# Kernel optimization log

Measured on AMD Instinct MI355X. Metric: run time of the kernel, lower is better.

## Reference

```python
import jax, jax.numpy as jnp
import numpy as np

B, N, A, M = 65536, 256, 64, 128  # frames, atoms, align atoms, nn atoms


def setup_inputs() -> dict:
    key = jax.random.key(0)
    k1, k2, k3, k4 = jax.random.split(key, 4)
    traj = jax.random.normal(k1, (B, N, 3), dtype=jnp.float32)
    ref_pos = jax.random.normal(k2, (N, 3), dtype=jnp.float32)
    align_idx = jnp.sort(jax.random.randint(k3, (A,), 0, N))
    nn_idx = jnp.sort(jax.random.randint(k4, (M,), 0, N))
    return {"traj": traj, "ref_pos": ref_pos, "align_idx": align_idx, "nn_idx": nn_idx}


def reference(traj, ref_pos, align_idx, nn_idx):
    # Reference structure: select alignment atoms and remove centroid (done once in __init__)
    ref_x = ref_pos[align_idx]                      # [A, 3]
    ref_x = ref_x - ref_x.mean(axis=0, keepdims=True)

    # Kabsch alignment per frame
    sel = traj[:, align_idx, :]                     # [B, A, 3]
    x_c = sel.mean(axis=1, keepdims=True)           # [B, 1, 3]
    x_notran = sel - x_c                            # [B, A, 3]
    # prod = x_notran^T @ ref_x -> [B, 3, 3]
    prod = jnp.einsum('bni,nj->bij', x_notran, ref_x)
    u, s, vh = jnp.linalg.svd(prod)                 # batched 3x3 SVD
    # proper-rotation sign correction (detached in original)
    sign = jax.lax.stop_gradient(jnp.sign(jnp.linalg.det(u @ vh)))  # [B]
    ones = jnp.ones_like(sign)
    d = jnp.stack([ones, ones, sign], axis=-1)      # [B, 3] diagonal of correction
    rot = (u * d[:, None, :]) @ vh                  # [B, 3, 3]

    # apply translation + rotation to ALL atoms
    aligned = jnp.einsum('bni,bij->bnj', traj - x_c, rot)  # [B, N, 3]

    # select NN input atoms and flatten
    return aligned[:, nn_idx, :].reshape(traj.shape[0], -1)  # [B, M*3]
```

## Files before the change

kernel.cpp:

```cpp
#include <hip/hip_runtime.h>

#define NB 65536
#define NATOM 256
#define NA 64
#define NM 128
#define TRAJ_SZ (NB*NATOM*3)
#define REF_SZ  (NATOM*3)
#define SLOT_F  384
#define ROW_F   (NATOM*3)

__device__ __forceinline__ float bf2f(unsigned short u) {
    union { unsigned int i; float f; } v; v.i = ((unsigned int)u) << 16; return v.f;
}
__device__ __forceinline__ float wave_sum(float v) {
    #pragma unroll
    for (int m = 1; m < 64; m <<= 1) v += __shfl_xor(v, m, 64);
    return v;
}
__device__ __forceinline__ float wave_max(float v) {
    #pragma unroll
    for (int m = 1; m < 64; m <<= 1) v = fmaxf(v, __shfl_xor(v, m, 64));
    return v;
}

__device__ __forceinline__ int detect_f32(const unsigned short* __restrict__ traj_u) {
    int lane = threadIdx.x & 63;
    float mx = fabsf(bf2f(traj_u[2 * lane]));
    mx = wave_max(mx);
    return (mx > 0.5f && mx < 100.f) ? 0 : 1;
}

__global__ __launch_bounds__(256) void k_fused(const unsigned short* __restrict__ traj_u,
                                               const unsigned short* __restrict__ refp_u,
                                               const int* __restrict__ align_idx,
                                               const int* __restrict__ nn_idx,
                                               float* __restrict__ out) {
    __shared__ float rowbuf[4][ROW_F];
    __shared__ float outbuf[4][SLOT_F];
    int lane = threadIdx.x & 63;
    int wid  = threadIdx.x >> 6;
    long batch = ((long)blockIdx.x << 2) + wid;
    int isf32 = detect_f32(traj_u);

    if (isf32) {
        const float4* src = (const float4*)((const float*)traj_u + batch * ROW_F);
        float4* dst = (float4*)rowbuf[wid];
        dst[lane]       = src[lane];
        dst[lane + 64]  = src[lane + 64];
        dst[lane + 128] = src[lane + 128];
    } else {
        const unsigned int* src = (const unsigned int*)(traj_u + batch * ROW_F);
        float2* dst = (float2*)rowbuf[wid];
        #pragma unroll
        for (int k = 0; k < 6; ++k) {
            unsigned int u = src[lane + 64 * k];
            dst[lane + 64 * k] = make_float2(bf2f((unsigned short)(u & 0xffffu)),
                                             bf2f((unsigned short)(u >> 16)));
        }
    }
    __syncthreads();

    int aidx = align_idx[lane];
    float r0, r1, r2;
    if (isf32) {
        const float* rp = (const float*)refp_u;
        r0 = rp[aidx*3+0]; r1 = rp[aidx*3+1]; r2 = rp[aidx*3+2];
    } else {
        r0 = bf2f(refp_u[aidx*3+0]); r1 = bf2f(refp_u[aidx*3+1]); r2 = bf2f(refp_u[aidx*3+2]);
    }
    float x0 = rowbuf[wid][aidx*3+0];
    float x1 = rowbuf[wid][aidx*3+1];
    float x2 = rowbuf[wid][aidx*3+2];
    r0 -= wave_sum(r0) * (1.f/64.f);
    r1 -= wave_sum(r1) * (1.f/64.f);
    r2 -= wave_sum(r2) * (1.f/64.f);
    float p00 = wave_sum(x0*r0), p01 = wave_sum(x0*r1), p02 = wave_sum(x0*r2);
    float p10 = wave_sum(x1*r0), p11 = wave_sum(x1*r1), p12 = wave_sum(x1*r2);
    float p20 = wave_sum(x2*r0), p21 = wave_sum(x2*r1), p22 = wave_sum(x2*r2);
    float xc0 = wave_sum(x0) * (1.f/64.f);
    float xc1 = wave_sum(x1) * (1.f/64.f);
    float xc2 = wave_sum(x2) * (1.f/64.f);

    float s00 = p00*p00 + p10*p10 + p20*p20;
    float s01 = p00*p01 + p10*p11 + p20*p21;
    float s02 = p00*p02 + p10*p12 + p20*p22;
    float s11 = p01*p01 + p11*p11 + p21*p21;
    float s12 = p01*p02 + p11*p12 + p21*p22;
    float s22 = p02*p02 + p12*p12 + p22*p22;
    float v00=1.f,v01=0.f,v02=0.f, v10=0.f,v11=1.f,v12=0.f, v20=0.f,v21=0.f,v22=1.f;
#define JROT(SPP,SQQ,SPQ,SRP,SRQ,VA,VB,VC,VD,VE,VF) { \
    float apq = SPQ; \
    if (apq != 0.0f) { \
        float tau = (SQQ - SPP) / (2.0f*apq); \
        float t = (tau >= 0.0f ? 1.0f : -1.0f) / (fabsf(tau) + sqrtf(1.0f + tau*tau)); \
        float c = 1.0f / sqrtf(1.0f + t*t); \
        float sn = t*c; \
        SPP -= t*apq; SQQ += t*apq; SPQ = 0.0f; \
        float tp = SRP; SRP = c*tp - sn*SRQ; SRQ = sn*tp + c*SRQ; \
        tp = VA; VA = c*tp - sn*VB; VB = sn*tp + c*VB; \
        tp = VC; VC = c*tp - sn*VD; VD = sn*tp + c*VD; \
        tp = VE; VE = c*tp - sn*VF; VF = sn*tp + c*VF; \
    } }
    #pragma unroll
    for (int sweep = 0; sweep < 5; ++sweep) {
        JROT(s00,s11,s01, s02,s12, v00,v01, v10,v11, v20,v21);
        JROT(s00,s22,s02, s01,s12, v00,v02, v10,v12, v20,v22);
        JROT(s11,s22,s12, s01,s02, v01,v02, v11,v12, v21,v22);
    }
#undef JROT
    float v1x,v1y,v1z, v2x,v2y,v2z;
    if (s00 <= s11 && s00 <= s22) {
        v1x=v01; v1y=v11; v1z=v21;  v2x=v02; v2y=v12; v2z=v22;
    } else if (s11 <= s22) {
        v1x=v02; v1y=v12; v1z=v22;  v2x=v00; v2y=v10; v2z=v20;
    } else {
        v1x=v00; v1y=v10; v1z=v20;  v2x=v01; v2y=v11; v2z=v21;
    }
    float u1x = p00*v1x + p01*v1y + p02*v1z;
    float u1y = p10*v1x + p11*v1y + p12*v1z;
    float u1z = p20*v1x + p21*v1y + p22*v1z;
    float inv = 1.0f / sqrtf(u1x*u1x + u1y*u1y + u1z*u1z);
    u1x*=inv; u1y*=inv; u1z*=inv;
    float u2x = p00*v2x + p01*v2y + p02*v2z;
    float u2y = p10*v2x + p11*v2y + p12*v2z;
    float u2z = p20*v2x + p21*v2y + p22*v2z;
    float d = u2x*u1x + u2y*u1y + u2z*u1z;
    u2x -= d*u1x; u2y -= d*u1y; u2z -= d*u1z;
    inv = 1.0f / sqrtf(u2x*u2x + u2y*u2y + u2z*u2z);
    u2x*=inv; u2y*=inv; u2z*=inv;
    float u3x = u1y*u2z - u1z*u2y;
    float u3y = u1z*u2x - u1x*u2z;
    float u3z = u1x*u2y - u1y*u2x;
    float v3x = v1y*v2z - v1z*v2y;
    float v3y = v1z*v2x - v1x*v2z;
    float v3z = v1x*v2y - v1y*v2x;
    float r00 = u1x*v1x + u2x*v2x + u3x*v3x;
    float r01 = u1x*v1y + u2x*v2y + u3x*v3y;
    float r02 = u1x*v1z + u2x*v2z + u3x*v3z;
    float r10 = u1y*v1x + u2y*v2x + u3y*v3x;
    float r11 = u1y*v1y + u2y*v2y + u3y*v3y;
    float r12 = u1y*v1z + u2y*v2z + u3y*v3z;
    float r20 = u1z*v1x + u2z*v2x + u3z*v3x;
    float r21 = u1z*v1y + u2z*v2y + u3z*v3y;
    float r22 = u1z*v1z + u2z*v2z + u3z*v3z;

    #pragma unroll
    for (int h = 0; h < 2; ++h) {
        int m = lane + 64 * h;
        int nidx = nn_idx[m];
        float y0 = rowbuf[wid][nidx*3+0] - xc0;
        float y1 = rowbuf[wid][nidx*3+1] - xc1;
        float y2 = rowbuf[wid][nidx*3+2] - xc2;
        outbuf[wid][3*m+0] = y0*r00 + y1*r10 + y2*r20;
        outbuf[wid][3*m+1] = y0*r01 + y1*r11 + y2*r21;
        outbuf[wid][3*m+2] = y0*r02 + y1*r12 + y2*r22;
    }
    __syncthreads();
    const float4* ob = (const float4*)outbuf[wid];
    float4* og = (float4*)(out + batch * SLOT_F);
    og[lane] = ob[lane];
    if (lane < 32) og[64 + lane] = ob[64 + lane];
}

extern "C" void kernel_launch(void* const* d_in, const int* in_sizes, int n_in,
                              void* d_out, int out_size, void* d_ws, size_t ws_size,
                              hipStream_t stream) {
    const unsigned short* traj = (const unsigned short*)d_in[0];
    const unsigned short* refp = (const unsigned short*)d_in[1];
    const int* align_idx = (const int*)d_in[2];
    const int* nn_idx    = (const int*)d_in[3];
    for (int i = 0; i < n_in; ++i) {
        if      (in_sizes[i] == TRAJ_SZ) traj      = (const unsigned short*)d_in[i];
        else if (in_sizes[i] == REF_SZ)  refp      = (const unsigned short*)d_in[i];
        else if (in_sizes[i] == NA)      align_idx = (const int*)d_in[i];
        else if (in_sizes[i] == NM)      nn_idx    = (const int*)d_in[i];
    }
    float* out = (float*)d_out;

    k_fused<<<NB/4, 256, 0, stream>>>(traj, refp, align_idx, nn_idx, out);
}
```

Baseline: 374.4 us.

## Batch eight frames per block and run the SVD once per frame across lanes

Each block now processes eight frames instead of four. Each wave reduces the cross-covariance for two frames, and the partial sums are staged in shared memory. A single lane per frame then runs the Jacobi eigen-solve and builds the rotation, where before all 64 lanes of a wave repeated the same 3x3 solve. The rotated output is written back in place over the row buffer and stored cooperatively by the whole block. The aim is to remove the redundant per-lane SVD work and the separate output buffer. The cost is two more block-wide barriers and a solve stage that runs on only eight lanes while the other waves sit idle.

Result: faster. 318.2 us (-15.0%).

```diff
diff --git a/kernel.cpp b/kernel.cpp
--- a/kernel.cpp
+++ b/kernel.cpp
@@ -8,6 +8,7 @@
 #define REF_SZ  (NATOM*3)
 #define SLOT_F  384
 #define ROW_F   (NATOM*3)
+#define NBB     8
 
 __device__ __forceinline__ float bf2f(unsigned short u) {
     union { unsigned int i; float f; } v; v.i = ((unsigned int)u) << 16; return v.f;
@@ -35,27 +36,27 @@
                                                const int* __restrict__ align_idx,
                                                const int* __restrict__ nn_idx,
                                                float* __restrict__ out) {
-    __shared__ float rowbuf[4][ROW_F];
-    __shared__ float outbuf[4][SLOT_F];
-    int lane = threadIdx.x & 63;
-    int wid  = threadIdx.x >> 6;
-    long batch = ((long)blockIdx.x << 2) + wid;
+    __shared__ float rowbuf[NBB][ROW_F];
+    __shared__ float pbuf[NBB][12];
+    int tid  = threadIdx.x;
+    int lane = tid & 63;
+    int wid  = tid >> 6;
+    long bbase = (long)blockIdx.x * NBB;
     int isf32 = detect_f32(traj_u);
 
     if (isf32) {
-        const float4* src = (const float4*)((const float*)traj_u + batch * ROW_F);
-        float4* dst = (float4*)rowbuf[wid];
-        dst[lane]       = src[lane];
-        dst[lane + 64]  = src[lane + 64];
-        dst[lane + 128] = src[lane + 128];
+        const float2* src = (const float2*)((const float*)traj_u + bbase * ROW_F);
+        float2* dst = (float2*)&rowbuf[0][0];
+        #pragma unroll
+        for (int k = 0; k < 12; ++k) dst[tid + 256*k] = src[tid + 256*k];
     } else {
-        const unsigned int* src = (const unsigned int*)(traj_u + batch * ROW_F);
-        float2* dst = (float2*)rowbuf[wid];
+        const unsigned int* src = (const unsigned int*)(traj_u + bbase * ROW_F);
+        float2* dst = (float2*)&rowbuf[0][0];
         #pragma unroll
-        for (int k = 0; k < 6; ++k) {
-            unsigned int u = src[lane + 64 * k];
-            dst[lane + 64 * k] = make_float2(bf2f((unsigned short)(u & 0xffffu)),
-                                             bf2f((unsigned short)(u >> 16)));
+        for (int k = 0; k < 12; ++k) {
+            unsigned int u = src[tid + 256*k];
+            dst[tid + 256*k] = make_float2(bf2f((unsigned short)(u & 0xffffu)),
+                                           bf2f((unsigned short)(u >> 16)));
         }
     }
     __syncthreads();
@@ -68,98 +69,142 @@
     } else {
         r0 = bf2f(refp_u[aidx*3+0]); r1 = bf2f(refp_u[aidx*3+1]); r2 = bf2f(refp_u[aidx*3+2]);
     }
-    float x0 = rowbuf[wid][aidx*3+0];
-    float x1 = rowbuf[wid][aidx*3+1];
-    float x2 = rowbuf[wid][aidx*3+2];
     r0 -= wave_sum(r0) * (1.f/64.f);
     r1 -= wave_sum(r1) * (1.f/64.f);
     r2 -= wave_sum(r2) * (1.f/64.f);
-    float p00 = wave_sum(x0*r0), p01 = wave_sum(x0*r1), p02 = wave_sum(x0*r2);
-    float p10 = wave_sum(x1*r0), p11 = wave_sum(x1*r1), p12 = wave_sum(x1*r2);
-    float p20 = wave_sum(x2*r0), p21 = wave_sum(x2*r1), p22 = wave_sum(x2*r2);
-    float xc0 = wave_sum(x0) * (1.f/64.f);
-    float xc1 = wave_sum(x1) * (1.f/64.f);
-    float xc2 = wave_sum(x2) * (1.f/64.f);
-
-    float s00 = p00*p00 + p10*p10 + p20*p20;
-    float s01 = p00*p01 + p10*p11 + p20*p21;
-    float s02 = p00*p02 + p10*p12 + p20*p22;
-    float s11 = p01*p01 + p11*p11 + p21*p21;
-    float s12 = p01*p02 + p11*p12 + p21*p22;
-    float s22 = p02*p02 + p12*p12 + p22*p22;
-    float v00=1.f,v01=0.f,v02=0.f, v10=0.f,v11=1.f,v12=0.f, v20=0.f,v21=0.f,v22=1.f;
+    #pragma unroll
+    for (int s = 0; s < 2; ++s) {
+        int lb = 2*wid + s;
+        const float* row = rowbuf[lb];
+        float x0 = row[aidx*3+0];
+        float x1 = row[aidx*3+1];
+        float x2 = row[aidx*3+2];
+        float p00 = wave_sum(x0*r0), p01 = wave_sum(x0*r1), p02 = wave_sum(x0*r2);
+        float p10 = wave_sum(x1*r0), p11 = wave_sum(x1*r1), p12 = wave_sum(x1*r2);
+        float p20 = wave_sum(x2*r0), p21 = wave_sum(x2*r1), p22 = wave_sum(x2*r2);
+        float xc0 = wave_sum(x0) * (1.f/64.f);
+        float xc1 = wave_sum(x1) * (1.f/64.f);
+        float xc2 = wave_sum(x2) * (1.f/64.f);
+        if (lane == 0) {
+            pbuf[lb][0] = p00; pbuf[lb][1] = p01; pbuf[lb][2]  = p02;
+            pbuf[lb][3] = p10; pbuf[lb][4] = p11; pbuf[lb][5]  = p12;
+            pbuf[lb][6] = p20; pbuf[lb][7] = p21; pbuf[lb][8]  = p22;
+            pbuf[lb][9] = xc0; pbuf[lb][10] = xc1; pbuf[lb][11] = xc2;
+        }
+    }
+    __syncthreads();
+
+    if (tid < NBB) {
+        float* w = pbuf[tid];
+        float p00=w[0], p01=w[1], p02=w[2];
+        float p10=w[3], p11=w[4], p12=w[5];
+        float p20=w[6], p21=w[7], p22=w[8];
+        float s00 = p00*p00 + p10*p10 + p20*p20;
+        float s01 = p00*p01 + p10*p11 + p20*p21;
+        float s02 = p00*p02 + p10*p12 + p20*p22;
+        float s11 = p01*p01 + p11*p11 + p21*p21;
+        float s12 = p01*p02 + p11*p12 + p21*p22;
+        float s22 = p02*p02 + p12*p12 + p22*p22;
+        float v00=1.f,v01=0.f,v02=0.f, v10=0.f,v11=1.f,v12=0.f, v20=0.f,v21=0.f,v22=1.f;
 #define JROT(SPP,SQQ,SPQ,SRP,SRQ,VA,VB,VC,VD,VE,VF) { \
-    float apq = SPQ; \
-    if (apq != 0.0f) { \
-        float tau = (SQQ - SPP) / (2.0f*apq); \
-        float t = (tau >= 0.0f ? 1.0f : -1.0f) / (fabsf(tau) + sqrtf(1.0f + tau*tau)); \
-        float c = 1.0f / sqrtf(1.0f + t*t); \
-        float sn = t*c; \
-        SPP -= t*apq; SQQ += t*apq; SPQ = 0.0f; \
-        float tp = SRP; SRP = c*tp - sn*SRQ; SRQ = sn*tp + c*SRQ; \
-        tp = VA; VA = c*tp - sn*VB; VB = sn*tp + c*VB; \
-        tp = VC; VC = c*tp - sn*VD; VD = sn*tp + c*VD; \
-        tp = VE; VE = c*tp - sn*VF; VF = sn*tp + c*VF; \
-    } }
-    #pragma unroll
-    for (int sweep = 0; sweep < 5; ++sweep) {
-        JROT(s00,s11,s01, s02,s12, v00,v01, v10,v11, v20,v21);
-        JROT(s00,s22,s02, s01,s12, v00,v02, v10,v12, v20,v22);
-        JROT(s11,s22,s12, s01,s02, v01,v02, v11,v12, v21,v22);
-    }
+        float apq = SPQ; \
+        if (apq != 0.0f) { \
+            float tau = (SQQ - SPP) / (2.0f*apq); \
+            float t = (tau >= 0.0f ? 1.0f : -1.0f) / (fabsf(tau) + sqrtf(1.0f + tau*tau)); \
+            float c = 1.0f / sqrtf(1.0f + t*t); \
+            float sn = t*c; \
+            SPP -= t*apq; SQQ += t*apq; SPQ = 0.0f; \
+            float tp = SRP; SRP = c*tp - sn*SRQ; SRQ = sn*tp + c*SRQ; \
+            tp = VA; VA = c*tp - sn*VB; VB = sn*tp + c*VB; \
+            tp = VC; VC = c*tp - sn*VD; VD = sn*tp + c*VD; \
+            tp = VE; VE = c*tp - sn*VF; VF = sn*tp + c*VF; \
+        } }
+        #pragma unroll
+        for (int sweep = 0; sweep < 5; ++sweep) {
+            JROT(s00,s11,s01, s02,s12, v00,v01, v10,v11, v20,v21);
+            JROT(s00,s22,s02, s01,s12, v00,v02, v10,v12, v20,v22);
+            JROT(s11,s22,s12, s01,s02, v01,v02, v11,v12, v21,v22);
+        }
 #undef JROT
-    float v1x,v1y,v1z, v2x,v2y,v2z;
-    if (s00 <= s11 && s00 <= s22) {
-        v1x=v01; v1y=v11; v1z=v21;  v2x=v02; v2y=v12; v2z=v22;
-    } else if (s11 <= s22) {
-        v1x=v02; v1y=v12; v1z=v22;  v2x=v00; v2y=v10; v2z=v20;
-    } else {
-        v1x=v00; v1y=v10; v1z=v20;  v2x=v01; v2y=v11; v2z=v21;
-    }
-    float u1x = p00*v1x + p01*v1y + p02*v1z;
-    float u1y = p10*v1x + p11*v1y + p12*v1z;
-    float u1z = p20*v1x + p21*v1y + p22*v1z;
-    float inv = 1.0f / sqrtf(u1x*u1x + u1y*u1y + u1z*u1z);
-    u1x*=inv; u1y*=inv; u1z*=inv;
-    float u2x = p00*v2x + p01*v2y + p02*v2z;
-    float u2y = p10*v2x + p11*v2y + p12*v2z;
-    float u2z = p20*v2x + p21*v2y + p22*v2z;
-    float d = u2x*u1x + u2y*u1y + u2z*u1z;
-    u2x -= d*u1x; u2y -= d*u1y; u2z -= d*u1z;
-    inv = 1.0f / sqrtf(u2x*u2x + u2y*u2y + u2z*u2z);
-    u2x*=inv; u2y*=inv; u2z*=inv;
-    float u3x = u1y*u2z - u1z*u2y;
-    float u3y = u1z*u2x - u1x*u2z;
-    float u3z = u1x*u2y - u1y*u2x;
-    float v3x = v1y*v2z - v1z*v2y;
-    float v3y = v1z*v2x - v1x*v2z;
-    float v3z = v1x*v2y - v1y*v2x;
-    float r00 = u1x*v1x + u2x*v2x + u3x*v3x;
-    float r01 = u1x*v1y + u2x*v2y + u3x*v3y;
-    float r02 = u1x*v1z + u2x*v2z + u3x*v3z;
-    float r10 = u1y*v1x + u2y*v2x + u3y*v3x;
-    float r11 = u1y*v1y + u2y*v2y + u3y*v3y;
-    float r12 = u1y*v1z + u2y*v2z + u3y*v3z;
-    float r20 = u1z*v1x + u2z*v2x + u3z*v3x;
-    float r21 = u1z*v1y + u2z*v2y + u3z*v3y;
-    float r22 = u1z*v1z + u2z*v2z + u3z*v3z;
-
-    #pragma unroll
-    for (int h = 0; h < 2; ++h) {
-        int m = lane + 64 * h;
-        int nidx = nn_idx[m];
-        float y0 = rowbuf[wid][nidx*3+0] - xc0;
-        float y1 = rowbuf[wid][nidx*3+1] - xc1;
-        float y2 = rowbuf[wid][nidx*3+2] - xc2;
-        outbuf[wid][3*m+0] = y0*r00 + y1*r10 + y2*r20;
-        outbuf[wid][3*m+1] = y0*r01 + y1*r11 + y2*r21;
-        outbuf[wid][3*m+2] = y0*r02 + y1*r12 + y2*r22;
-    }
-    __syncthreads();
-    const float4* ob = (const float4*)outbuf[wid];
-    float4* og = (float4*)(out + batch * SLOT_F);
-    og[lane] = ob[lane];
-    if (lane < 32) og[64 + lane] = ob[64 + lane];
+        float v1x,v1y,v1z, v2x,v2y,v2z;
+        if (s00 <= s11 && s00 <= s22) {
+            v1x=v01; v1y=v11; v1z=v21;  v2x=v02; v2y=v12; v2z=v22;
+        } else if (s11 <= s22) {
+            v1x=v02; v1y=v12; v1z=v22;  v2x=v00; v2y=v10; v2z=v20;
+        } else {
+            v1x=v00; v1y=v10; v1z=v20;  v2x=v01; v2y=v11; v2z=v21;
+        }
+        float u1x = p00*v1x + p01*v1y + p02*v1z;
+        float u1y = p10*v1x + p11*v1y + p12*v1z;
+        float u1z = p20*v1x + p21*v1y + p22*v1z;
+        float inv = 1.0f / sqrtf(u1x*u1x + u1y*u1y + u1z*u1z);
+        u1x*=inv; u1y*=inv; u1z*=inv;
+        float u2x = p00*v2x + p01*v2y + p02*v2z;
+        float u2y = p10*v2x + p11*v2y + p12*v2z;
+        float u2z = p20*v2x + p21*v2y + p22*v2z;
+        float d = u2x*u1x + u2y*u1y + u2z*u1z;
+        u2x -= d*u1x; u2y -= d*u1y; u2z -= d*u1z;
+        inv = 1.0f / sqrtf(u2x*u2x + u2y*u2y + u2z*u2z);
+        u2x*=inv; u2y*=inv; u2z*=inv;
+        float u3x = u1y*u2z - u1z*u2y;
+        float u3y = u1z*u2x - u1x*u2z;
+        float u3z = u1x*u2y - u1y*u2x;
+        float v3x = v1y*v2z - v1z*v2y;
+        float v3y = v1z*v2x - v1x*v2z;
+        float v3z = v1x*v2y - v1y*v2x;
+        w[0] = u1x*v1x + u2x*v2x + u3x*v3x;
+        w[1] = u1x*v1y + u2x*v2y + u3x*v3y;
+        w[2] = u1x*v1z + u2x*v2z + u3x*v3z;
+        w[3] = u1y*v1x + u2y*v2x + u3y*v3x;
+        w[4] = u1y*v1y + u2y*v2y + u3y*v3y;
+        w[5] = u1y*v1z + u2y*v2z + u3y*v3z;
+        w[6] = u1z*v1x + u2z*v2x + u3z*v3x;
+        w[7] = u1z*v1y + u2z*v2y + u3z*v3y;
+        w[8] = u1z*v1z + u2z*v2z + u3z*v3z;
+    }
+    __syncthreads();
+
+    int n0 = nn_idx[lane];
+    int n1 = nn_idx[lane + 64];
+    #pragma unroll
+    for (int s = 0; s < 2; ++s) {
+        int lb = 2*wid + s;
+        float* row = rowbuf[lb];
+        const float* w = pbuf[lb];
+        float r00=w[0], r01=w[1], r02=w[2];
+        float r10=w[3], r11=w[4], r12=w[5];
+        float r20=w[6], r21=w[7], r22=w[8];
+        float xc0=w[9], xc1=w[10], xc2=w[11];
+        float a0 = row[n0*3+0] - xc0;
+        float a1 = row[n0*3+1] - xc1;
+        float a2 = row[n0*3+2] - xc2;
+        float b0 = row[n1*3+0] - xc0;
+        float b1 = row[n1*3+1] - xc1;
+        float b2 = row[n1*3+2] - xc2;
+        float o0 = a0*r00 + a1*r10 + a2*r20;
+        float o1 = a0*r01 + a1*r11 + a2*r21;
+        float o2 = a0*r02 + a1*r12 + a2*r22;
+        float o3 = b0*r00 + b1*r10 + b2*r20;
+        float o4 = b0*r01 + b1*r11 + b2*r21;
+        float o5 = b0*r02 + b1*r12 + b2*r22;
+        row[3*lane+0] = o0;
+        row[3*lane+1] = o1;
+        row[3*lane+2] = o2;
+        row[3*(lane+64)+0] = o3;
+        row[3*(lane+64)+1] = o4;
+        row[3*(lane+64)+2] = o5;
+    }
+    __syncthreads();
+
+    float4* og = (float4*)(out + bbase * SLOT_F);
+    const float4* ob = (const float4*)&rowbuf[0][0];
+    #pragma unroll
+    for (int k = 0; k < 3; ++k) {
+        int idx = tid + 256*k;
+        int b = idx / 96;
+        int o = idx - b*96;
+        og[idx] = ob[b*192 + o];
+    }
 }
 
 extern "C" void kernel_launch(void* const* d_in, const int* in_sizes, int n_in,
@@ -177,5 +222,5 @@
     }
     float* out = (float*)d_out;
 
-    k_fused<<<NB/4, 256, 0, stream>>>(traj, refp, align_idx, nn_idx, out);
-}
+    k_fused<<<NB/NBB, 256, 0, stream>>>(traj, refp, align_idx, nn_idx, out);
+}
```
